# Kernel optimization log

Hardware: AMD Instinct MI355X
Metric: run time of the kernel (lower is better)

The kernel has to match this reference:

```python
import jax, jax.numpy as jnp
import numpy as np

M_RANGE = 5
K = 2 * M_RANGE + 1      # 11
N_CLASS = K * K          # 121
IM_CHANNEL = 3


def _gconv(x, w, groups):
    # torch F.conv2d(x, w, None, stride=1, padding=M_RANGE, dilation=1, groups)
    return jax.lax.conv_general_dilated(
        x, w, window_strides=(1, 1),
        padding=[(M_RANGE, M_RANGE)] * 2,
        dimension_numbers=('NCHW', 'OIHW', 'NCHW'),
        feature_group_count=groups)


def setup_inputs() -> dict:
    key = jax.random.key(0)
    k1, k2 = jax.random.split(key)
    B, H, W = 8, 128, 128
    im_input = jax.random.normal(k1, (B, 2 * IM_CHANNEL, H, W), jnp.float32)
    # motion in [-m_range, m_range-1) so idx and idx+1 stay in [0, K-1]
    gt_motion = jax.random.uniform(k2, (B, 2, H, W), jnp.float32,
                                   minval=-float(M_RANGE), maxval=float(M_RANGE - 1) - 1e-3)
    # canonical one-hot displacement kernels, [n_class, 1, K, K] (torch OIHW after swapaxes)
    m_kernel = jnp.eye(N_CLASS, dtype=jnp.float32).reshape(N_CLASS, 1, K, K)
    return {"im_input": im_input, "gt_motion": gt_motion, "m_kernel": m_kernel}


def motion2mask(motion):
    # vectorized version of the per-pixel bilinear one-hot construction
    mf = jnp.floor(motion)
    frac = motion - mf                              # [B,2,H,W]
    idx = mf.astype(jnp.int32) + M_RANGE            # [B,2,H,W]
    grid = jnp.arange(K)[None, :, None, None]       # [1,K,1,1]

    def onehot(i, f):                               # i,f: [B,H,W] -> [B,K,H,W]
        i = i[:, None]
        f = f[:, None]
        return jnp.where(grid == i, 1.0 - f, 0.0) + jnp.where(grid == i + 1, f, 0.0)

    a = onehot(idx[:, 0], frac[:, 0])               # x-axis weights
    b = onehot(idx[:, 1], frac[:, 1])               # y-axis weights
    B, _, H, W = motion.shape
    # torch.ger(b, a).view(-1): channel = by*K + ax
    return (b[:, :, None] * a[:, None, :]).reshape(B, N_CLASS, H, W)


def reference(im_input, gt_motion, m_kernel):
    B, _, H, W = gt_motion.shape
    m_mask = motion2mask(gt_motion)                          # [B,C,H,W]
    out_mask = _gconv(m_mask, m_kernel, N_CLASS)             # [B,C,H,W]
    # construct_seg
    ones = jnp.ones_like(out_mask)
    seg = (_gconv(ones, m_kernel, N_CLASS) * out_mask).sum(1)  # [B,H,W]
    appear = jax.nn.relu(1.0 - seg)
    disappear = jax.nn.relu(seg - 1.0)
    # construct_image
    im = im_input[:, -IM_CHANNEL:] * (1.0 - disappear)[:, None]   # [B,ch,H,W]
    im_exp = jnp.repeat(im, N_CLASS, axis=1)                      # [B,ch*C,H,W]
    w_tiled = jnp.tile(m_kernel, (IM_CHANNEL, 1, 1, 1))           # [ch*C,1,K,K]
    nearby = _gconv(im_exp, w_tiled, IM_CHANNEL * N_CLASS)
    nearby = nearby.reshape(B, IM_CHANNEL, N_CLASS, H, W)
    pred = (nearby * out_mask[:, None]).sum(2)                    # [B,ch,H,W]
    return pred, m_mask, disappear, appear
```

## Files before the change

kernel.cpp:

```cpp
#include <hip/hip_runtime.h>

#define HW       16384
#define NCLASS   121

#define OFF_PRED 0
#define OFF_MASK (8 * 3 * HW)
#define OFF_DIS  (OFF_MASK + 8 * NCLASS * HW)
#define OFF_APP  (OFF_DIS + 8 * HW)

#define NSEGBLK  256
#define NPREDBLK 768
#define NMASKBLK (8 * 16 * 11)

__device__ __forceinline__ float hatf(float u) { return fmaxf(0.f, 1.f - fabsf(u)); }

__global__ __launch_bounds__(256) void k_seg(const float* __restrict__ motion,
                                             float* __restrict__ out) {
    __shared__ float sseg[4 * 128];
    int blk = blockIdx.x;
    int b   = blk >> 5;
    int y0  = (blk & 31) << 2;
    int tid = threadIdx.x;

    const float* motx = motion + (size_t)(b * 2) * HW;
    const float* moty = motx + HW;

    ((float2*)sseg)[tid] = make_float2(0.f, 0.f);
    __syncthreads();
    #pragma unroll
    for (int it = 0; it < 7; ++it) {
        int idx = tid + it * 256;
        int sy  = y0 - 5 + (idx >> 7);
        int sx  = idx & 127;
        if (sy >= 0 && sy < 128) {
            int s = sy * 128 + sx;
            float mx = motx[s], my = moty[s];
            float flx = floorf(mx), fly = floorf(my);
            float fa = mx - flx, fb = my - fly;
            int ia = (int)flx + 5, ib = (int)fly + 5;
            float wa0 = 1.f - fa, wa1 = fa;
            float wb0 = 1.f - fb, wb1 = fb;
            #pragma unroll
            for (int j = 0; j < 2; ++j) {
                int ty = sy - (ib + j) + 5;
                if (ty < y0 || ty >= y0 + 4) continue;
                float wb = j ? wb1 : wb0;
                #pragma unroll
                for (int i = 0; i < 2; ++i) {
                    int tx = sx - (ia + i) + 5;
                    if (tx < 0 || tx >= 128) continue;
                    atomicAdd(&sseg[(ty - y0) * 128 + tx], wb * (i ? wa1 : wa0));
                }
            }
        }
    }
    __syncthreads();
    int p2 = tid * 2;
    int ly = p2 >> 7;
    int x  = p2 & 127;
    float2 s2 = *(float2*)&sseg[ly * 128 + x];
    float2 d2, a2;
    d2.x = fmaxf(s2.x - 1.f, 0.f); a2.x = fmaxf(1.f - s2.x, 0.f);
    d2.y = fmaxf(s2.y - 1.f, 0.f); a2.y = fmaxf(1.f - s2.y, 0.f);
    int p = b * HW + (y0 + ly) * 128 + x;
    *(float2*)(out + OFF_DIS + p) = d2;
    *(float2*)(out + OFF_APP + p) = a2;
}

__global__ __launch_bounds__(256) void k_maskpred(const float* __restrict__ motion,
                                                  const float* __restrict__ im_input,
                                                  float* __restrict__ out) {
    __shared__ float spred[4 * 128];
    int tid = threadIdx.x;
    int blk = blockIdx.x;

    if (blk < NPREDBLK) {
        int c  = blk >> 8;
        int t  = blk & 255;
        int b  = t >> 5;
        int y0 = (t & 31) << 2;
        const float* motx = motion + (size_t)(b * 2) * HW;
        const float* moty = motx + HW;
        const float* imc  = im_input + (size_t)(b * 6 + 3 + c) * HW;
        const float* disb = out + OFF_DIS + (size_t)b * HW;

        ((float2*)spred)[tid] = make_float2(0.f, 0.f);
        __syncthreads();

        #pragma unroll
        for (int it = 0; it < 7; ++it) {
            int idx = tid + it * 256;
            int sy  = y0 - 5 + (idx >> 7);
            int sx  = idx & 127;
            if (sy >= 0 && sy < 128) {
                int s = sy * 128 + sx;
                float mx = motx[s], my = moty[s];
                float iv = imc[s] * (1.f - disb[s]);
                float flx = floorf(mx), fly = floorf(my);
                float fa = mx - flx, fb = my - fly;
                int ia = (int)flx + 5, ib = (int)fly + 5;
                float wa0 = 1.f - fa, wa1 = fa;
                float wb0 = 1.f - fb, wb1 = fb;
                #pragma unroll
                for (int j = 0; j < 2; ++j) {
                    int ty = sy - (ib + j) + 5;
                    if (ty < y0 || ty >= y0 + 4) continue;
                    float wb = j ? wb1 : wb0;
                    #pragma unroll
                    for (int i = 0; i < 2; ++i) {
                        int tx = sx - (ia + i) + 5;
                        if (tx < 0 || tx >= 128) continue;
                        atomicAdd(&spred[(ty - y0) * 128 + tx], wb * (i ? wa1 : wa0) * iv);
                    }
                }
            }
        }
        __syncthreads();

        int p2 = tid * 2;
        int ly = p2 >> 7;
        int x  = p2 & 127;
        float2 v = *(float2*)&spred[ly * 128 + x];
        float* predb = out + OFF_PRED + (size_t)(b * 3 + c) * HW + (y0 + ly) * 128 + x;
        *(float2*)predb = v;
    } else {
        int mb = blk - NPREDBLK;
        int kb = mb % 11;
        int tl = mb / 11;
        int b  = tl >> 4;
        int y0 = (tl & 15) << 3;
        const float* motx = motion + (size_t)(b * 2) * HW;
        const float* moty = motx + HW;

        int ly = tid >> 5;
        int x4 = (tid & 31) << 2;
        int g  = (y0 + ly) * 128 + x4;
        float4 mx = *(const float4*)(motx + g);
        float4 my = *(const float4*)(moty + g);
        float kbo = (float)(kb - 5);
        float4 bv;
        bv.x = hatf(my.x - kbo); bv.y = hatf(my.y - kbo);
        bv.z = hatf(my.z - kbo); bv.w = hatf(my.w - kbo);
        float* mm = out + OFF_MASK + ((size_t)(b * NCLASS + kb * 11)) * HW + g;
        #pragma unroll
        for (int ka = 0; ka < 11; ++ka) {
            float kao = (float)(ka - 5);
            float4 v;
            v.x = bv.x * hatf(mx.x - kao);
            v.y = bv.y * hatf(mx.y - kao);
            v.z = bv.z * hatf(mx.z - kao);
            v.w = bv.w * hatf(mx.w - kao);
            *(float4*)(mm + (size_t)ka * HW) = v;
        }
    }
}

extern "C" void kernel_launch(void* const* d_in, const int* in_sizes, int n_in,
                              void* d_out, int out_size, void* d_ws, size_t ws_size,
                              hipStream_t stream) {
    const float* im_input = (const float*)d_in[0];
    const float* motion   = (const float*)d_in[1];
    float* out = (float*)d_out;

    k_seg<<<dim3(NSEGBLK), dim3(256), 0, stream>>>(motion, out);
    k_maskpred<<<dim3(NPREDBLK + NMASKBLK), dim3(256), 0, stream>>>(motion, im_input, out);
}
```

Before: 23.58 us.

## Shrink row tiles, fuse mask writes into pred blocks, use nontemporal stores

The seg kernel now handles one output row per block, and the pred kernel two rows per block with more blocks, so the halo loads are spread across more CUs. The separate mask-writing blocks are gone: each pred block also writes a slice of the 121-channel mask for its two rows, spreading the large mask store traffic evenly. Loads are hoisted into registers with sentinel values before the atomic scatter, and outputs use nontemporal stores. The cost is more redundant halo loading, since each source row is read by more blocks.

```diff
diff --git a/kernel.cpp b/kernel.cpp
--- a/kernel.cpp
+++ b/kernel.cpp
@@ -8,150 +8,166 @@
 #define OFF_DIS  (OFF_MASK + 8 * NCLASS * HW)
 #define OFF_APP  (OFF_DIS + 8 * HW)
 
-#define NSEGBLK  256
-#define NPREDBLK 768
-#define NMASKBLK (8 * 16 * 11)
+#define SENT 100000.0f
+
+typedef float nfloat4 __attribute__((ext_vector_type(4)));
 
 __device__ __forceinline__ float hatf(float u) { return fmaxf(0.f, 1.f - fabsf(u)); }
+__device__ __forceinline__ void nt4(float* p, float a, float b, float c, float d) {
+    nfloat4 v; v.x = a; v.y = b; v.z = c; v.w = d;
+    __builtin_nontemporal_store(v, (nfloat4*)p);
+}
 
 __global__ __launch_bounds__(256) void k_seg(const float* __restrict__ motion,
                                              float* __restrict__ out) {
-    __shared__ float sseg[4 * 128];
+    __shared__ float sseg[128];
+    int tid = threadIdx.x;
     int blk = blockIdx.x;
-    int b   = blk >> 5;
-    int y0  = (blk & 31) << 2;
-    int tid = threadIdx.x;
+    int b   = blk >> 7;
+    int y0  = blk & 127;
 
     const float* motx = motion + (size_t)(b * 2) * HW;
     const float* moty = motx + HW;
 
-    ((float2*)sseg)[tid] = make_float2(0.f, 0.f);
-    __syncthreads();
+    float mxv[6], myv[6];
     #pragma unroll
-    for (int it = 0; it < 7; ++it) {
+    for (int it = 0; it < 6; ++it) {
         int idx = tid + it * 256;
         int sy  = y0 - 5 + (idx >> 7);
         int sx  = idx & 127;
-        if (sy >= 0 && sy < 128) {
-            int s = sy * 128 + sx;
-            float mx = motx[s], my = moty[s];
-            float flx = floorf(mx), fly = floorf(my);
-            float fa = mx - flx, fb = my - fly;
-            int ia = (int)flx + 5, ib = (int)fly + 5;
-            float wa0 = 1.f - fa, wa1 = fa;
-            float wb0 = 1.f - fb, wb1 = fb;
+        bool ok = (idx < 1408) && (sy >= 0) && (sy < 128);
+        int s   = (ok ? sy : 0) * 128 + sx;
+        float a = motx[s], bb = moty[s];
+        mxv[it] = ok ? a : SENT;
+        myv[it] = ok ? bb : SENT;
+    }
+
+    if (tid < 128) sseg[tid] = 0.f;
+    __syncthreads();
+
+    #pragma unroll
+    for (int it = 0; it < 6; ++it) {
+        int idx = tid + it * 256;
+        int sy  = y0 - 5 + (idx >> 7);
+        int sx  = idx & 127;
+        float mx = mxv[it], my = myv[it];
+        float flx = floorf(mx), fly = floorf(my);
+        float fa = mx - flx, fb = my - fly;
+        int ia = (int)flx + 5, ib = (int)fly + 5;
+        float wa0 = 1.f - fa, wa1 = fa, wb0 = 1.f - fb, wb1 = fb;
+        #pragma unroll
+        for (int j = 0; j < 2; ++j) {
+            int ty = sy - (ib + j) + 5;
+            if (ty != y0) continue;
+            float wb = j ? wb1 : wb0;
             #pragma unroll
-            for (int j = 0; j < 2; ++j) {
-                int ty = sy - (ib + j) + 5;
-                if (ty < y0 || ty >= y0 + 4) continue;
-                float wb = j ? wb1 : wb0;
-                #pragma unroll
-                for (int i = 0; i < 2; ++i) {
-                    int tx = sx - (ia + i) + 5;
-                    if (tx < 0 || tx >= 128) continue;
-                    atomicAdd(&sseg[(ty - y0) * 128 + tx], wb * (i ? wa1 : wa0));
-                }
+            for (int i = 0; i < 2; ++i) {
+                int tx = sx - (ia + i) + 5;
+                if (tx < 0 || tx >= 128) continue;
+                atomicAdd(&sseg[tx], wb * (i ? wa1 : wa0));
             }
         }
     }
     __syncthreads();
-    int p2 = tid * 2;
-    int ly = p2 >> 7;
-    int x  = p2 & 127;
-    float2 s2 = *(float2*)&sseg[ly * 128 + x];
-    float2 d2, a2;
-    d2.x = fmaxf(s2.x - 1.f, 0.f); a2.x = fmaxf(1.f - s2.x, 0.f);
-    d2.y = fmaxf(s2.y - 1.f, 0.f); a2.y = fmaxf(1.f - s2.y, 0.f);
-    int p = b * HW + (y0 + ly) * 128 + x;
-    *(float2*)(out + OFF_DIS + p) = d2;
-    *(float2*)(out + OFF_APP + p) = a2;
+
+    if (tid < 128) {
+        float v = sseg[tid];
+        int p = b * HW + y0 * 128 + tid;
+        out[OFF_DIS + p] = fmaxf(v - 1.f, 0.f);
+        out[OFF_APP + p] = fmaxf(1.f - v, 0.f);
+    }
 }
 
-__global__ __launch_bounds__(256) void k_maskpred(const float* __restrict__ motion,
+__global__ __launch_bounds__(256) void k_predmask(const float* __restrict__ motion,
                                                   const float* __restrict__ im_input,
                                                   float* __restrict__ out) {
-    __shared__ float spred[4 * 128];
+    __shared__ float spred[2 * 128];
     int tid = threadIdx.x;
     int blk = blockIdx.x;
+    int c   = blk % 3;
+    int t   = blk / 3;
+    int b   = t >> 6;
+    int y0  = (t & 63) << 1;
 
-    if (blk < NPREDBLK) {
-        int c  = blk >> 8;
-        int t  = blk & 255;
-        int b  = t >> 5;
-        int y0 = (t & 31) << 2;
-        const float* motx = motion + (size_t)(b * 2) * HW;
-        const float* moty = motx + HW;
-        const float* imc  = im_input + (size_t)(b * 6 + 3 + c) * HW;
-        const float* disb = out + OFF_DIS + (size_t)b * HW;
+    const float* motx = motion + (size_t)(b * 2) * HW;
+    const float* moty = motx + HW;
+    const float* imc  = im_input + (size_t)(b * 6 + 3 + c) * HW;
+    const float* disb = out + OFF_DIS + (size_t)b * HW;
 
-        ((float2*)spred)[tid] = make_float2(0.f, 0.f);
-        __syncthreads();
+    int cell = tid & 63;
+    int mly  = cell >> 5;
+    int mx4  = (cell & 31) << 2;
+    int gC   = (y0 + mly) * 128 + mx4;
+    float4 cmx = *(const float4*)(motx + gC);
+    float4 cmy = *(const float4*)(moty + gC);
 
+    float mxv[6], myv[6], imv[6], dsv[6];
+    #pragma unroll
+    for (int it = 0; it < 6; ++it) {
+        int idx = tid + it * 256;
+        int sy  = y0 - 5 + (idx >> 7);
+        int sx  = idx & 127;
+        bool ok = (sy >= 0) && (sy < 128);
+        int s   = (ok ? sy : 0) * 128 + sx;
+        float a = motx[s], bb = moty[s], cc = imc[s], dd = disb[s];
+        mxv[it] = ok ? a : SENT;
+        myv[it] = ok ? bb : SENT;
+        imv[it] = ok ? cc : 0.f;
+        dsv[it] = ok ? dd : 0.f;
+    }
+
+    spred[tid] = 0.f;
+    __syncthreads();
+
+    {
+        int s0  = c * 4 + (tid >> 6);
+        int ch0 = (s0 * 121) / 12;
+        int ch1 = ((s0 + 1) * 121) / 12;
+        float* mmB = out + OFF_MASK + (size_t)(b * NCLASS) * HW + gC;
+        for (int ch = ch0; ch < ch1; ++ch) {
+            int kb = ch / 11;
+            int ka = ch - kb * 11;
+            float kao = (float)(ka - 5), kbo = (float)(kb - 5);
+            nt4(mmB + (size_t)ch * HW,
+                hatf(cmy.x - kbo) * hatf(cmx.x - kao),
+                hatf(cmy.y - kbo) * hatf(cmx.y - kao),
+                hatf(cmy.z - kbo) * hatf(cmx.z - kao),
+                hatf(cmy.w - kbo) * hatf(cmx.w - kao));
+        }
+    }
+
+    #pragma unroll
+    for (int it = 0; it < 6; ++it) {
+        int idx = tid + it * 256;
+        int sy  = y0 - 5 + (idx >> 7);
+        int sx  = idx & 127;
+        float mx = mxv[it], my = myv[it];
+        float iv = imv[it] * (1.f - dsv[it]);
+        float flx = floorf(mx), fly = floorf(my);
+        float fa = mx - flx, fb = my - fly;
+        int ia = (int)flx + 5, ib = (int)fly + 5;
+        float wa0 = 1.f - fa, wa1 = fa, wb0 = 1.f - fb, wb1 = fb;
         #pragma unroll
-        for (int it = 0; it < 7; ++it) {
-            int idx = tid + it * 256;
-            int sy  = y0 - 5 + (idx >> 7);
-            int sx  = idx & 127;
-            if (sy >= 0 && sy < 128) {
-                int s = sy * 128 + sx;
-                float mx = motx[s], my = moty[s];
-                float iv = imc[s] * (1.f - disb[s]);
-                float flx = floorf(mx), fly = floorf(my);
-                float fa = mx - flx, fb = my - fly;
-                int ia = (int)flx + 5, ib = (int)fly + 5;
-                float wa0 = 1.f - fa, wa1 = fa;
-                float wb0 = 1.f - fb, wb1 = fb;
-                #pragma unroll
-                for (int j = 0; j < 2; ++j) {
-                    int ty = sy - (ib + j) + 5;
-                    if (ty < y0 || ty >= y0 + 4) continue;
-                    float wb = j ? wb1 : wb0;
-                    #pragma unroll
-                    for (int i = 0; i < 2; ++i) {
-                        int tx = sx - (ia + i) + 5;
-                        if (tx < 0 || tx >= 128) continue;
-                        atomicAdd(&spred[(ty - y0) * 128 + tx], wb * (i ? wa1 : wa0) * iv);
-                    }
-                }
+        for (int j = 0; j < 2; ++j) {
+            int ty = sy - (ib + j) + 5;
+            if (ty < y0 || ty >= y0 + 2) continue;
+            float wb = j ? wb1 : wb0;
+            #pragma unroll
+            for (int i = 0; i < 2; ++i) {
+                int tx = sx - (ia + i) + 5;
+                if (tx < 0 || tx >= 128) continue;
+                atomicAdd(&spred[(ty - y0) * 128 + tx], wb * (i ? wa1 : wa0) * iv);
             }
         }
-        __syncthreads();
+    }
+    __syncthreads();
 
-        int p2 = tid * 2;
-        int ly = p2 >> 7;
-        int x  = p2 & 127;
-        float2 v = *(float2*)&spred[ly * 128 + x];
-        float* predb = out + OFF_PRED + (size_t)(b * 3 + c) * HW + (y0 + ly) * 128 + x;
-        *(float2*)predb = v;
-    } else {
-        int mb = blk - NPREDBLK;
-        int kb = mb % 11;
-        int tl = mb / 11;
-        int b  = tl >> 4;
-        int y0 = (tl & 15) << 3;
-        const float* motx = motion + (size_t)(b * 2) * HW;
-        const float* moty = motx + HW;
-
-        int ly = tid >> 5;
-        int x4 = (tid & 31) << 2;
-        int g  = (y0 + ly) * 128 + x4;
-        float4 mx = *(const float4*)(motx + g);
-        float4 my = *(const float4*)(moty + g);
-        float kbo = (float)(kb - 5);
-        float4 bv;
-        bv.x = hatf(my.x - kbo); bv.y = hatf(my.y - kbo);
-        bv.z = hatf(my.z - kbo); bv.w = hatf(my.w - kbo);
-        float* mm = out + OFF_MASK + ((size_t)(b * NCLASS + kb * 11)) * HW + g;
-        #pragma unroll
-        for (int ka = 0; ka < 11; ++ka) {
-            float kao = (float)(ka - 5);
-            float4 v;
-            v.x = bv.x * hatf(mx.x - kao);
-            v.y = bv.y * hatf(mx.y - kao);
-            v.z = bv.z * hatf(mx.z - kao);
-            v.w = bv.w * hatf(mx.w - kao);
-            *(float4*)(mm + (size_t)ka * HW) = v;
-        }
+    {
+        int ly = tid >> 7;
+        int x  = tid & 127;
+        __builtin_nontemporal_store(
+            spred[tid],
+            out + OFF_PRED + (size_t)(b * 3 + c) * HW + (y0 + ly) * 128 + x);
     }
 }
 
@@ -162,6 +178,6 @@
     const float* motion   = (const float*)d_in[1];
     float* out = (float*)d_out;
 
-    k_seg<<<dim3(NSEGBLK), dim3(256), 0, stream>>>(motion, out);
-    k_maskpred<<<dim3(NPREDBLK + NMASKBLK), dim3(256), 0, stream>>>(motion, im_input, out);
+    k_seg<<<dim3(1024), dim3(256), 0, stream>>>(motion, out);
+    k_predmask<<<dim3(1536), dim3(256), 0, stream>>>(motion, im_input, out);
 }
```

After: 23.59 us. About the same (+0.0%).
